# Optimization experiments

Measured on AMD Instinct MI355X. Metric: run time of the kernel, lower is better.

Reference implementation:

```python
import jax, jax.numpy as jnp
import numpy as np

C, P, G = 80, 30000, 800       # classes, preds/class, gts/class
IOU_THR = 0.5
IMG = 1024.0                   # synthetic image size
BATCH = 16                     # images per batch (box[0] = image index)


def _make_boxes(key, n_cls, n):
    """Boxes in the module's 7-col layout: [img_idx, class, score, x1, y1, x2, y2]."""
    k1, k2, k3, k4 = jax.random.split(key, 4)
    xy = jax.random.uniform(k1, (n_cls, n, 2), minval=0.0, maxval=IMG - 128.0)
    wh = jax.random.uniform(k2, (n_cls, n, 2), minval=4.0, maxval=128.0)
    score = jax.random.uniform(k3, (n_cls, n, 1))
    img_idx = jax.random.randint(k4, (n_cls, n, 1), 0, BATCH).astype(jnp.float32)
    cls = jnp.zeros((n_cls, n, 1), jnp.float32)
    return jnp.concatenate([img_idx, cls, score, xy, xy + wh], axis=-1)


def setup_inputs() -> dict:
    key = jax.random.key(0)
    kp, kg = jax.random.split(key)
    return {"pred_boxes": _make_boxes(kp, C, P), "gt_boxes": _make_boxes(kg, C, G)}


def _pairwise_iou(a, b):
    # a: [P,4], b: [G,4] corner-format xyxy -> [P,G]
    lt = jnp.maximum(a[:, None, :2], b[None, :, :2])
    rb = jnp.minimum(a[:, None, 2:], b[None, :, 2:])
    wh = jnp.clip(rb - lt, 0.0)
    inter = wh[..., 0] * wh[..., 1]
    area_a = (a[:, 2] - a[:, 0]) * (a[:, 3] - a[:, 1])
    area_b = (b[:, 2] - b[:, 0]) * (b[:, 3] - b[:, 1])
    return inter / (area_a[:, None] + area_b[None, :] - inter + 1e-9)


def _ap_one_class(pb, gb):
    # pb: [P,7] preds, gb: [G,7] gts for one class
    n_p, n_g = pb.shape[0], gb.shape[0]
    order = jnp.argsort(-pb[:, 2])             # sort preds by score desc
    boxes = pb[order, 3:7]
    iou = _pairwise_iou(boxes, gb[:, 3:7])     # [P,G]
    best_iou = iou.max(axis=1)
    match = iou.argmax(axis=1)                 # best gt per pred
    valid = best_iou > IOU_THR
    p_idx = jnp.arange(n_p, dtype=jnp.int32)
    # first (highest-score) valid pred claiming each gt -> TP; later claims -> FP
    first = jnp.full((n_g,), n_p, jnp.int32).at[match].min(
        jnp.where(valid, p_idx, n_p))
    tp = (valid & (p_idx == first[match])).astype(jnp.float32)
    ctp = jnp.cumsum(tp)
    cfp = jnp.cumsum(1.0 - tp)
    recall = ctp / (n_g + 1e-9)
    precision = ctp / (ctp + cfp + 1e-9)
    # trapezoidal AP over the PR curve (torch.trapz(precisions, recalls))
    return jnp.sum((recall[1:] - recall[:-1]) * (precision[1:] + precision[:-1]) * 0.5)


def reference(pred_boxes, gt_boxes):
    # sequential map over classes keeps peak memory at one [P,G] IoU matrix
    aps = jax.lax.map(lambda ab: _ap_one_class(ab[0], ab[1]), (pred_boxes, gt_boxes))
    return jnp.mean(aps)
```

## Files before the change

### kernel.cpp

```cpp
#include <hip/hip_runtime.h>

#define C 80
#define P 30000
#define G 800
#define BS 256
#define NB 16
#define NC (NB * NB)
#define PPT 8
#define TPB (BS * PPT)
#define HCH 8
#define CHSZ ((P + HCH - 1) / HCH)


__device__ __forceinline__ unsigned long long pack_key(float s, int p) {
    return ((unsigned long long)__float_as_uint(s) << 32) | (unsigned)(P - 1 - p);
}

__device__ __forceinline__ int cell_coord(float v) {
    return min(max((int)(v * (1.0f / 64.0f)), 0), NB - 1);
}

__device__ __forceinline__ int cell_of_center(float cxf, float cyf) {
    return cell_coord(cyf) * NB + cell_coord(cxf);
}

__global__ __launch_bounds__(BS) void gt_bin_kernel(
        const float* __restrict__ gt,
        unsigned short* __restrict__ gtCnt, unsigned short* __restrict__ gtOff,
        float4* __restrict__ gtBox, float* __restrict__ gtAbe,
        unsigned short* __restrict__ gtIdx,
        unsigned long long* __restrict__ gtKey, int* __restrict__ gHist,
        unsigned int* __restrict__ doneCnt) {
    __shared__ int h[NC], cur[NC];
    __shared__ int gcell[G];
    const int c = blockIdx.x, tid = threadIdx.x;
    h[tid] = 0;
    if (c == 0 && tid == 0) *doneCnt = 0u;
    for (int i = tid; i < G; i += BS) gtKey[c * G + i] = 0ull;
    for (int j = tid; j < 1024; j += BS) gHist[c * 1024 + j] = 0;
    __syncthreads();
    for (int i = tid; i < G; i += BS) {
        const float* r = gt + ((size_t)c * G + i) * 7;
        int cl = cell_of_center(0.5f * (r[3] + r[5]), 0.5f * (r[4] + r[6]));
        gcell[i] = cl;
        atomicAdd(&h[cl], 1);
    }
    __syncthreads();
    const int v = h[tid];
    cur[tid] = v;
    __syncthreads();
    for (int o = 1; o < NC; o <<= 1) {
        int t = (tid >= o) ? cur[tid - o] : 0;
        __syncthreads();
        cur[tid] += t;
        __syncthreads();
    }
    const int excl = cur[tid] - v;
    gtOff[c * NC + tid] = (unsigned short)excl;
    gtCnt[c * NC + tid] = (unsigned short)v;
    __syncthreads();
    cur[tid] = excl;
    __syncthreads();
    for (int i = tid; i < G; i += BS) {
        const float* r = gt + ((size_t)c * G + i) * 7;
        float x1 = r[3], y1 = r[4], x2 = r[5], y2 = r[6];
        int slot = atomicAdd(&cur[gcell[i]], 1);
        gtBox[c * G + slot] = make_float4(x1, y1, x2, y2);
        gtAbe[c * G + slot] = __fadd_rn(__fmul_rn(__fsub_rn(x2, x1), __fsub_rn(y2, y1)), 1e-9f);
        gtIdx[c * G + slot] = (unsigned short)i;
    }
}

__global__ __launch_bounds__(BS) void match8_kernel(
        const float* __restrict__ pred,
        const unsigned short* __restrict__ gtOff, const unsigned short* __restrict__ gtCnt,
        const float4* __restrict__ gtBox, const float* __restrict__ gtAbe,
        const unsigned short* __restrict__ gtIdx,
        unsigned long long* __restrict__ gtKey) {
    __shared__ float4 sB[G];
    __shared__ float  sE[G];
    __shared__ unsigned short sG[G];
    __shared__ unsigned short sOff[NC], sCnt[NC];
    __shared__ unsigned short sIdx[TPB];
    __shared__ int hcnt[NC], bb[NC];
    const int c = blockIdx.y, tid = threadIdx.x;
    const int p0 = blockIdx.x * TPB;
    const int cntP = min(TPB, P - p0);

    for (int i = tid; i < G; i += BS) {
        sB[i] = gtBox[c * G + i];
        sE[i] = gtAbe[c * G + i];
        sG[i] = gtIdx[c * G + i];
    }
    sOff[tid] = gtOff[c * NC + tid];
    sCnt[tid] = gtCnt[c * NC + tid];
    hcnt[tid] = 0;
    __syncthreads();

    const size_t cp = (size_t)c * P;

    unsigned char  cellA[PPT];
    unsigned short lrA[PPT];
    #pragma unroll
    for (int rep = 0; rep < PPT; ++rep) {
        const int li = rep * BS + tid;
        const int p  = p0 + li;
        int cell = 0, lr = 0;
        if (p < P) {
            const float* r = pred + (cp + p) * 7;
            cell = cell_of_center(0.5f * (r[3] + r[5]), 0.5f * (r[4] + r[6]));
            lr = atomicAdd(&hcnt[cell], 1);
        }
        cellA[rep] = (unsigned char)cell;
        lrA[rep] = (unsigned short)lr;
    }
    __syncthreads();

    const int v = hcnt[tid];
    __syncthreads();
    for (int o = 1; o < NC; o <<= 1) {
        int t = (tid >= o) ? hcnt[tid - o] : 0;
        __syncthreads();
        hcnt[tid] += t;
        __syncthreads();
    }
    bb[tid] = hcnt[tid] - v;
    __syncthreads();

    #pragma unroll
    for (int rep = 0; rep < PPT; ++rep) {
        const int li = rep * BS + tid;
        if (p0 + li < P) sIdx[bb[cellA[rep]] + lrA[rep]] = (unsigned short)li;
    }
    __syncthreads();

    #pragma unroll 1
    for (int rep = 0; rep < PPT; ++rep) {
        const int si = rep * BS + tid;
        if (si < cntP) {
            const int li = sIdx[si];
            const int p  = p0 + li;
            const float* r = pred + (cp + p) * 7;
            float ax1 = r[3], ay1 = r[4], ax2 = r[5], ay2 = r[6];
            float A = __fmul_rn(__fsub_rn(ax2, ax1), __fsub_rn(ay2, ay1));
            const int x0 = cell_coord(ax1), x1 = cell_coord(ax2);
            const int y0 = cell_coord(ay1), y1 = cell_coord(ay2);
            float IN = 0.0f, SB = 1.0f;
            int mj = -1;
            for (int yy = y0; yy <= y1; ++yy) {
                const int rowb = yy * NB;
                const int jb = sOff[rowb + x0];
                const int je = sOff[rowb + x1] + sCnt[rowb + x1];
                #pragma unroll 2
                for (int j = jb; j < je; ++j) {
                    float4 b = sB[j];
                    float lx = fmaxf(ax1, b.x), ly = fmaxf(ay1, b.y);
                    float rx = fminf(ax2, b.z), ry = fminf(ay2, b.w);
                    float wx = fmaxf(__fsub_rn(rx, lx), 0.0f);
                    float wy = fmaxf(__fsub_rn(ry, ly), 0.0f);
                    float in = __fmul_rn(wx, wy);
                    float sb = __fadd_rn(A, sE[j]);
                    bool  up = __fmul_rn(in, SB) > __fmul_rn(IN, sb);
                    IN = up ? in : IN; SB = up ? sb : SB; mj = up ? j : mj;
                }
            }
            if (IN > 0.0f) {
                float4 b = sB[mj];
                float area = __fmul_rn(__fsub_rn(b.z, b.x), __fsub_rn(b.w, b.y));
                float dn = __fadd_rn(__fsub_rn(__fadd_rn(A, area), IN), 1e-9f);
                float iou = __fdiv_rn(IN, dn);
                if (iou > 0.5f) {
                    float sscore = r[2];
                    atomicMax(&gtKey[c * G + sG[mj]], pack_key(sscore, p));
                }
            }
        }
    }
}

__global__ __launch_bounds__(BS) void histf_kernel(
        const float* __restrict__ pred,
        const unsigned long long* __restrict__ gtKey,
        int* __restrict__ gHist, int* __restrict__ sortT) {
    __shared__ unsigned long long k[G];
    __shared__ unsigned long long sk[1024];
    __shared__ int h[1024];
    __shared__ int cnt;
    const int c = blockIdx.y, chunk = blockIdx.x, tid = threadIdx.x;

    if (tid == 0) cnt = 0;
    for (int j = tid; j < 1024; j += BS) { sk[j] = 0ull; h[j] = 0; }
    __syncthreads();
    for (int i = tid; i < G; i += BS) {
        unsigned long long key = gtKey[c * G + i];
        if (key != 0ull) k[atomicAdd(&cnt, 1)] = key;
    }
    __syncthreads();
    const int T = cnt;
    if (chunk == 0 && tid == 0) sortT[c] = T;

    for (int t = tid; t < T; t += BS) {
        unsigned long long key = k[t];
        int pos = 0;
        for (int u = 0; u < T; ++u) pos += (k[u] > key) ? 1 : 0;
        sk[pos] = key;
    }
    __syncthreads();

    const int start = chunk * CHSZ;
    const int end   = min(start + CHSZ, P);
    const float* pr = pred + (size_t)c * P * 7;
    for (int i = start + tid; i < end; i += BS) {
        unsigned long long kq =
            ((unsigned long long)__float_as_uint(pr[(size_t)i * 7 + 2]) << 32)
            | (unsigned)(P - 1 - i);
        int lo = 0;
        #pragma unroll
        for (int step = 512; step > 0; step >>= 1)
            if (sk[lo + step - 1] > kq) lo += step;
        atomicAdd(&h[lo], 1);
    }
    __syncthreads();
    for (int j = tid; j < 1024; j += BS)
        if (h[j]) atomicAdd(&gHist[c * 1024 + j], h[j]);
}

__global__ __launch_bounds__(BS) void ap2m_kernel(
        const int* __restrict__ sortT, const int* __restrict__ gHist,
        float* __restrict__ ap, unsigned int* __restrict__ doneCnt,
        float* __restrict__ out) {
    __shared__ int ha[1024];
    __shared__ int hb[1024];
    __shared__ float red[BS];
    const int c = blockIdx.x, tid = threadIdx.x;
    const int T = sortT[c];
    for (int j = tid; j < 1024; j += BS) ha[j] = gHist[c * 1024 + j];
    __syncthreads();
    int* src = ha; int* dst = hb;
    for (int o = 1; o < 1024; o <<= 1) {
        for (int j = tid; j < 1024; j += BS)
            dst[j] = src[j] + ((j >= o) ? src[j - o] : 0);
        __syncthreads();
        int* tmp = src; src = dst; dst = tmp;
    }
    float sum = 0.0f;
    for (int s = tid; s < T; s += BS) {
        int r = src[s] - 1;
        if (r >= 1) {
            float kf  = (float)(s + 1);
            float km  = (float)s;
            float ri  = __fdiv_rn(kf, 800.0f);
            float rim = __fdiv_rn(km, 800.0f);
            float pi  = __fdiv_rn(kf, (float)(r + 1));
            float pim = __fdiv_rn(km, (float)r);
            sum = __fadd_rn(sum,
                  __fmul_rn(__fmul_rn(__fsub_rn(ri, rim), __fadd_rn(pi, pim)), 0.5f));
        }
    }
    red[tid] = sum;
    __syncthreads();
    for (int s2 = BS / 2; s2 > 0; s2 >>= 1) {
        if (tid < s2) red[tid] = __fadd_rn(red[tid], red[tid + s2]);
        __syncthreads();
    }
    if (tid == 0) {
        ap[c] = red[0];
        __threadfence();
        unsigned int t = atomicAdd(doneCnt, 1u);
        if (t == C - 1) {
            __threadfence();
            float s = 0.0f;
            for (int c2 = 0; c2 < C; ++c2) s = __fadd_rn(s, ap[c2]);
            out[0] = __fdiv_rn(s, 80.0f);
        }
    }
}

extern "C" void kernel_launch(void* const* d_in, const int* in_sizes, int n_in,
                              void* d_out, int out_size, void* d_ws, size_t ws_size,
                              hipStream_t stream) {
    const float* pred = (const float*)d_in[0];
    const float* gt   = (const float*)d_in[1];
    float* out = (float*)d_out;

    char* ws = (char*)d_ws;
    int*                sortT      = (int*)               (ws + 0);
    float*              ap         = (float*)             (ws + 512);
    unsigned int*       doneCnt    = (unsigned int*)      (ws + 896);
    unsigned short*     gtCnt      = (unsigned short*)    (ws + 1024);
    unsigned short*     gtOff      = (unsigned short*)    (ws + 41984);
    unsigned short*     gtIdx      = (unsigned short*)    (ws + 82944);
    float*              gtAbe      = (float*)             (ws + 210944);
    float4*             gtBox      = (float4*)            (ws + 466944);
    unsigned long long* gtKey      = (unsigned long long*)(ws + 1490944);
    int*                gHist      = (int*)               (ws + 2002944);

    const int M_BLK = (P + TPB - 1) / TPB;

    gt_bin_kernel<<<C, BS, 0, stream>>>(gt, gtCnt, gtOff, gtBox, gtAbe, gtIdx,
                                        gtKey, gHist, doneCnt);
    match8_kernel<<<dim3(M_BLK, C), BS, 0, stream>>>(pred, gtOff, gtCnt, gtBox,
                                                     gtAbe, gtIdx, gtKey);
    histf_kernel<<<dim3(HCH, C), BS, 0, stream>>>(pred, gtKey, gHist, sortT);
    ap2m_kernel<<<C, BS, 0, stream>>>(sortT, gHist, ap, doneCnt, out);
}
```

Measured before the change: 227.6 us.

## Bin predictions per class globally before matching instead of per-block sorting

Moves the spatial binning of predictions out of the match kernel into two new kernels: one computes each prediction's grid cell and a per-class cell histogram, and the other scatters prediction indices into a class-wide cell-sorted order. The match kernel then reads predictions in that global cell order, so neighbouring threads look at the same GT cells across the whole class rather than only within a 2048-prediction tile, which should reduce divergence and wasted IoU work. The cost is two extra kernel launches, extra global traffic for the cell and index arrays, and global atomics. The order within a cell is not deterministic, but this should not change the result because matches are resolved with score keys.

```diff
diff --git a/kernel.cpp b/kernel.cpp
--- a/kernel.cpp
+++ b/kernel.cpp
@@ -6,8 +6,8 @@
 #define BS 256
 #define NB 16
 #define NC (NB * NB)
-#define PPT 8
-#define TPB (BS * PPT)
+#define PPTM 8
+#define TPBM (BS * PPTM)
 #define HCH 8
 #define CHSZ ((P + HCH - 1) / HCH)
 
@@ -30,11 +30,14 @@
         float4* __restrict__ gtBox, float* __restrict__ gtAbe,
         unsigned short* __restrict__ gtIdx,
         unsigned long long* __restrict__ gtKey, int* __restrict__ gHist,
+        int* __restrict__ predCnt, int* __restrict__ predCur,
         unsigned int* __restrict__ doneCnt) {
     __shared__ int h[NC], cur[NC];
     __shared__ int gcell[G];
     const int c = blockIdx.x, tid = threadIdx.x;
     h[tid] = 0;
+    predCnt[c * NC + tid] = 0;
+    predCur[c * NC + tid] = 0;
     if (c == 0 && tid == 0) *doneCnt = 0u;
     for (int i = tid; i < G; i += BS) gtKey[c * G + i] = 0ull;
     for (int j = tid; j < 1024; j += BS) gHist[c * 1024 + j] = 0;
@@ -71,8 +74,53 @@
     }
 }
 
-__global__ __launch_bounds__(BS) void match8_kernel(
-        const float* __restrict__ pred,
+__global__ __launch_bounds__(BS) void pprep_kernel(
+        const float* __restrict__ pred, int* __restrict__ predCnt,
+        unsigned char* __restrict__ cellB) {
+    __shared__ int h[NC];
+    const int c = blockIdx.y, tid = threadIdx.x;
+    h[tid] = 0;
+    __syncthreads();
+    int p = blockIdx.x * BS + tid;
+    if (p < P) {
+        const float* r = pred + ((size_t)c * P + p) * 7;
+        int cl = cell_of_center(0.5f * (r[3] + r[5]), 0.5f * (r[4] + r[6]));
+        cellB[(size_t)c * P + p] = (unsigned char)cl;
+        atomicAdd(&h[cl], 1);
+    }
+    __syncthreads();
+    if (h[tid]) atomicAdd(&predCnt[c * NC + tid], h[tid]);
+}
+
+__global__ __launch_bounds__(BS) void pscatter_kernel(
+        const unsigned char* __restrict__ cellB, const int* __restrict__ predCnt,
+        int* __restrict__ predCur, unsigned short* __restrict__ pIdxS) {
+    __shared__ int h[NC], base[NC], sc[NC];
+    const int c = blockIdx.y, tid = threadIdx.x;
+    h[tid] = 0;
+    sc[tid] = predCnt[c * NC + tid];
+    const int v = sc[tid];
+    __syncthreads();
+    int p = blockIdx.x * BS + tid;
+    int cellv = 0, lr = 0;
+    if (p < P) {
+        cellv = cellB[(size_t)c * P + p];
+        lr = atomicAdd(&h[cellv], 1);
+    }
+    __syncthreads();
+    for (int o = 1; o < NC; o <<= 1) {
+        int t = (tid >= o) ? sc[tid - o] : 0;
+        __syncthreads();
+        sc[tid] += t;
+        __syncthreads();
+    }
+    if (h[tid]) base[tid] = (sc[tid] - v) + atomicAdd(&predCur[c * NC + tid], h[tid]);
+    __syncthreads();
+    if (p < P) pIdxS[(size_t)c * P + base[cellv] + lr] = (unsigned short)p;
+}
+
+__global__ __launch_bounds__(BS) void match10_kernel(
+        const float* __restrict__ pred, const unsigned short* __restrict__ pIdxS,
         const unsigned short* __restrict__ gtOff, const unsigned short* __restrict__ gtCnt,
         const float4* __restrict__ gtBox, const float* __restrict__ gtAbe,
         const unsigned short* __restrict__ gtIdx,
@@ -81,11 +129,8 @@
     __shared__ float  sE[G];
     __shared__ unsigned short sG[G];
     __shared__ unsigned short sOff[NC], sCnt[NC];
-    __shared__ unsigned short sIdx[TPB];
-    __shared__ int hcnt[NC], bb[NC];
     const int c = blockIdx.y, tid = threadIdx.x;
-    const int p0 = blockIdx.x * TPB;
-    const int cntP = min(TPB, P - p0);
+    const int s0 = blockIdx.x * TPBM;
 
     for (int i = tid; i < G; i += BS) {
         sB[i] = gtBox[c * G + i];
@@ -94,52 +139,14 @@
     }
     sOff[tid] = gtOff[c * NC + tid];
     sCnt[tid] = gtCnt[c * NC + tid];
-    hcnt[tid] = 0;
     __syncthreads();
 
     const size_t cp = (size_t)c * P;
-
-    unsigned char  cellA[PPT];
-    unsigned short lrA[PPT];
-    #pragma unroll
-    for (int rep = 0; rep < PPT; ++rep) {
-        const int li = rep * BS + tid;
-        const int p  = p0 + li;
-        int cell = 0, lr = 0;
-        if (p < P) {
-            const float* r = pred + (cp + p) * 7;
-            cell = cell_of_center(0.5f * (r[3] + r[5]), 0.5f * (r[4] + r[6]));
-            lr = atomicAdd(&hcnt[cell], 1);
-        }
-        cellA[rep] = (unsigned char)cell;
-        lrA[rep] = (unsigned short)lr;
-    }
-    __syncthreads();
-
-    const int v = hcnt[tid];
-    __syncthreads();
-    for (int o = 1; o < NC; o <<= 1) {
-        int t = (tid >= o) ? hcnt[tid - o] : 0;
-        __syncthreads();
-        hcnt[tid] += t;
-        __syncthreads();
-    }
-    bb[tid] = hcnt[tid] - v;
-    __syncthreads();
-
-    #pragma unroll
-    for (int rep = 0; rep < PPT; ++rep) {
-        const int li = rep * BS + tid;
-        if (p0 + li < P) sIdx[bb[cellA[rep]] + lrA[rep]] = (unsigned short)li;
-    }
-    __syncthreads();
-
     #pragma unroll 1
-    for (int rep = 0; rep < PPT; ++rep) {
-        const int si = rep * BS + tid;
-        if (si < cntP) {
-            const int li = sIdx[si];
-            const int p  = p0 + li;
+    for (int rep = 0; rep < PPTM; ++rep) {
+        const int slot = s0 + rep * BS + tid;
+        if (slot < P) {
+            const int p = pIdxS[cp + slot];
             const float* r = pred + (cp + p) * 7;
             float ax1 = r[3], ay1 = r[4], ax2 = r[5], ay2 = r[6];
             float A = __fmul_rn(__fsub_rn(ax2, ax1), __fsub_rn(ay2, ay1));
@@ -287,20 +294,27 @@
     int*                sortT      = (int*)               (ws + 0);
     float*              ap         = (float*)             (ws + 512);
     unsigned int*       doneCnt    = (unsigned int*)      (ws + 896);
-    unsigned short*     gtCnt      = (unsigned short*)    (ws + 1024);
-    unsigned short*     gtOff      = (unsigned short*)    (ws + 41984);
-    unsigned short*     gtIdx      = (unsigned short*)    (ws + 82944);
-    float*              gtAbe      = (float*)             (ws + 210944);
-    float4*             gtBox      = (float4*)            (ws + 466944);
-    unsigned long long* gtKey      = (unsigned long long*)(ws + 1490944);
-    int*                gHist      = (int*)               (ws + 2002944);
-
-    const int M_BLK = (P + TPB - 1) / TPB;
+    int*                predCnt    = (int*)               (ws + 1024);
+    int*                predCur    = (int*)               (ws + 82944);
+    unsigned short*     gtCnt      = (unsigned short*)    (ws + 164864);
+    unsigned short*     gtOff      = (unsigned short*)    (ws + 205824);
+    unsigned short*     gtIdx      = (unsigned short*)    (ws + 246784);
+    float*              gtAbe      = (float*)             (ws + 374784);
+    float4*             gtBox      = (float4*)            (ws + 630784);
+    unsigned long long* gtKey      = (unsigned long long*)(ws + 1654784);
+    int*                gHist      = (int*)               (ws + 2166784);
+    unsigned char*      cellB      = (unsigned char*)     (ws + 2494464);
+    unsigned short*     pIdxS      = (unsigned short*)    (ws + 4894464);
+
+    const int P_BLK = (P + BS - 1) / BS;
+    const int M_BLK = (P + TPBM - 1) / TPBM;
 
     gt_bin_kernel<<<C, BS, 0, stream>>>(gt, gtCnt, gtOff, gtBox, gtAbe, gtIdx,
-                                        gtKey, gHist, doneCnt);
-    match8_kernel<<<dim3(M_BLK, C), BS, 0, stream>>>(pred, gtOff, gtCnt, gtBox,
-                                                     gtAbe, gtIdx, gtKey);
+                                        gtKey, gHist, predCnt, predCur, doneCnt);
+    pprep_kernel<<<dim3(P_BLK, C), BS, 0, stream>>>(pred, predCnt, cellB);
+    pscatter_kernel<<<dim3(P_BLK, C), BS, 0, stream>>>(cellB, predCnt, predCur, pIdxS);
+    match10_kernel<<<dim3(M_BLK, C), BS, 0, stream>>>(pred, pIdxS, gtOff, gtCnt,
+                                                      gtBox, gtAbe, gtIdx, gtKey);
     histf_kernel<<<dim3(HCH, C), BS, 0, stream>>>(pred, gtKey, gHist, sortT);
     ap2m_kernel<<<C, BS, 0, stream>>>(sortT, gHist, ap, doneCnt, out);
 }
```

Result: slower. 257.1 us (+13.0%).
